# Kernel optimization log

Hardware: AMD Instinct MI355X
Metric: run time of the kernel (lower is better)

Reference implementation:

```python
import jax, jax.numpy as jnp
import numpy as np

N_NODES = 50000
N_EDGES = 1600000
D_IN = 128
D_HID = 128
D_OUT = 128


def setup_inputs() -> dict:
    key = jax.random.key(0)
    ks = jax.random.split(key, 12)
    s = 0.05
    return {
        "x": jax.random.normal(ks[0], (N_NODES, D_IN), jnp.float32),
        "src": jax.random.randint(ks[1], (N_EDGES,), 0, N_NODES),
        "dst": jax.random.randint(ks[2], (N_EDGES,), 0, N_NODES),
        "W_neigh1": jax.random.normal(ks[3], (D_HID, D_IN), jnp.float32) * s,
        "W_self1": jax.random.normal(ks[4], (D_HID, D_IN), jnp.float32) * s,
        "b_self1": jnp.zeros((D_HID,), jnp.float32),
        "W_neigh2": jax.random.normal(ks[5], (D_HID, D_HID), jnp.float32) * s,
        "W_self2": jax.random.normal(ks[6], (D_HID, D_HID), jnp.float32) * s,
        "b_self2": jnp.zeros((D_HID,), jnp.float32),
        "W_neigh3": jax.random.normal(ks[7], (D_OUT, D_HID), jnp.float32) * s,
        "W_self3": jax.random.normal(ks[8], (D_OUT, D_HID), jnp.float32) * s,
        "b_self3": jnp.zeros((D_OUT,), jnp.float32),
    }


def _sage_mean(h, src, dst, inv_deg, W_neigh, W_self, b_self):
    # DGL SAGEConv 'mean': fc_self(h) + fc_neigh(mean of in-neighbor feats)
    # zero in-degree nodes get zero neighbor term (inv_deg = 0 there is avoided
    # by clamping degree to >=1, sum is 0 anyway).
    neigh_sum = jax.ops.segment_sum(h[src], dst, num_segments=h.shape[0])  # [N, d]
    h_neigh = neigh_sum * inv_deg  # [N, d]
    return h @ W_self.T + b_self + h_neigh @ W_neigh.T


def reference(x, src, dst, W_neigh1, W_self1, b_self1, W_neigh2, W_self2, b_self2, W_neigh3, W_self3, b_self3):
    n = x.shape[0]
    deg = jax.ops.segment_sum(jnp.ones((src.shape[0],), x.dtype), dst, num_segments=n)
    inv_deg = (1.0 / jnp.maximum(deg, 1.0))[:, None]  # [N, 1]
    h = jax.nn.relu(_sage_mean(x, src, dst, inv_deg, W_neigh1, W_self1, b_self1))
    h = jax.nn.relu(_sage_mean(h, src, dst, inv_deg, W_neigh2, W_self2, b_self2))
    h = _sage_mean(h, src, dst, inv_deg, W_neigh3, W_self3, b_self3)
    return h
```

## Files before the change

kernel.cpp:

```cpp
#include <hip/hip_runtime.h>


constexpr int N_NODES = 50000;
constexpr int N_EDGES = 1600000;
constexpr int D = 128;
constexpr int NTILES = N_NODES / 16;

constexpr int NBUCK = 392;
constexpr int BCAP  = 6144;
constexpr int EPB   = 4096;
constexpr int CS_BLOCKS = (N_EDGES + EPB - 1) / EPB;
constexpr int GC_STRIDE = 16;

constexpr int NT  = 8;
constexpr int TSH = 13;

typedef __bf16 bf16x8 __attribute__((ext_vector_type(8)));
typedef float f32x4 __attribute__((ext_vector_type(4)));
union U8 { bf16x8 v; __bf16 e[8]; };

__global__ __launch_bounds__(256) void bucket_count_scatter(
        const int* __restrict__ dst, const int* __restrict__ src,
        int* __restrict__ gcursor, int* __restrict__ bucketbuf) {
    __shared__ int hcnt[NBUCK];
    __shared__ int hbase[NBUCK];
    const int tid = threadIdx.x;
    for (int i = tid; i < NBUCK; i += 256) hcnt[i] = 0;
    __syncthreads();

    const int e0 = blockIdx.x * EPB;
    int d[16], lp[16];
    #pragma unroll
    for (int t = 0; t < 16; ++t) {
        const int e = e0 + t * 256 + tid;
        if (e < N_EDGES) {
            d[t] = dst[e];
            lp[t] = atomicAdd(&hcnt[d[t] >> 7], 1);
        } else {
            d[t] = 0; lp[t] = -1;
        }
    }
    __syncthreads();

    for (int i = tid; i < NBUCK; i += 256) {
        const int c = hcnt[i];
        hbase[i] = c ? atomicAdd(&gcursor[i * GC_STRIDE], c) : 0;
    }
    __syncthreads();

    #pragma unroll
    for (int t = 0; t < 16; ++t) {
        const int e = e0 + t * 256 + tid;
        if (e < N_EDGES) {
            const int s  = src[e];
            const int bk = d[t] >> 7;
            const int p  = hbase[bk] + lp[t];
            if (p < BCAP)
                bucketbuf[bk * BCAP + p] = ((d[t] & 127) << 16) | s;
        }
    }
}

__global__ __launch_bounds__(256) void bucket_csr(
        const int* __restrict__ gcursor, const int* __restrict__ bucketbuf,
        int* __restrict__ tp, float* __restrict__ inv_deg,
        int* __restrict__ esrc) {
    __shared__ int h[1024];
    __shared__ int cur[1024];
    __shared__ int wsum[4], wpre[4];
    __shared__ int redw[4];
    const int bk = blockIdx.x, tid = threadIdx.x;
    int cnt = gcursor[bk * GC_STRIDE];
    if (cnt > BCAP) cnt = BCAP;

    int partial = 0;
    for (int i = tid; i < bk; i += 256) {
        int v = gcursor[i * GC_STRIDE];
        partial += (v > BCAP ? BCAP : v);
    }
    #pragma unroll
    for (int off = 32; off; off >>= 1) partial += __shfl_down(partial, off, 64);
    if ((tid & 63) == 0) redw[tid >> 6] = partial;

    #pragma unroll
    for (int k = 0; k < 4; ++k) h[tid * 4 + k] = 0;
    __syncthreads();
    const int base = redw[0] + redw[1] + redw[2] + redw[3];

    const int* bb = bucketbuf + (size_t)bk * BCAP;
    for (int i = tid; i < cnt; i += 256) {
        const int p = bb[i];
        atomicAdd(&h[((p >> 16) << 3) | ((p & 0xFFFF) >> TSH)], 1);
    }
    __syncthreads();

    if (tid < 128) {
        int dg = 0;
        #pragma unroll
        for (int k = 0; k < 8; ++k) dg += h[tid * 8 + k];
        inv_deg[bk * 128 + tid] = 1.0f / fmaxf((float)dg, 1.0f);
    }

    const int v0 = h[tid * 4], v1 = h[tid * 4 + 1];
    const int v2 = h[tid * 4 + 2], v3 = h[tid * 4 + 3];
    const int s = v0 + v1 + v2 + v3;
    int x = s;
    const int lane = tid & 63, w = tid >> 6;
    #pragma unroll
    for (int off = 1; off < 64; off <<= 1) {
        int tt = __shfl_up(x, off, 64);
        if (lane >= off) x += tt;
    }
    if (lane == 63) wsum[w] = x;
    __syncthreads();
    if (tid == 0) {
        int a = 0;
        #pragma unroll
        for (int k = 0; k < 4; ++k) { wpre[k] = a; a += wsum[k]; }
    }
    __syncthreads();
    const int e0 = wpre[w] + (x - s);
    const int e1 = e0 + v0, e2 = e1 + v1, e3 = e2 + v2;
    cur[tid * 4] = e0; cur[tid * 4 + 1] = e1;
    cur[tid * 4 + 2] = e2; cur[tid * 4 + 3] = e3;
    int* tpo = tp + (size_t)bk * 1024 + tid * 4;
    tpo[0] = base + e0; tpo[1] = base + e1; tpo[2] = base + e2; tpo[3] = base + e3;
    __syncthreads();

    for (int i = tid; i < cnt; i += 256) {
        const int p = bb[i];
        const int f = ((p >> 16) << 3) | ((p & 0xFFFF) >> TSH);
        esrc[base + atomicAdd(&cur[f], 1)] = p & 0xFFFF;
    }
}

__global__ void pack_w(const float* __restrict__ w0, const float* __restrict__ w1,
                       const float* __restrict__ w2, const float* __restrict__ w3,
                       const float* __restrict__ w4, const float* __restrict__ w5,
                       __bf16* __restrict__ outbase) {
    const float* ws[6] = {w0, w1, w2, w3, w4, w5};
    const float* W = ws[blockIdx.y];
    __bf16* o = outbase + (size_t)blockIdx.y * 32768;
    int idx = blockIdx.x * 256 + threadIdx.x;
    int t = idx & 7;
    int lane = (idx >> 3) & 63;
    int ks = (idx >> 9) & 3;
    int jt = idx >> 11;
    int j = jt * 16 + (lane & 15);
    int k = ks * 32 + (lane >> 4) * 8 + t;
    float w = W[j * D + k];
    __bf16 hi = (__bf16)w;
    o[idx] = hi;
    o[16384 + idx] = (__bf16)(w - (float)hi);
}

__global__ __launch_bounds__(256) void split_x(const float* __restrict__ x,
                                               __bf16* __restrict__ xh, int n8) {
    const int i = blockIdx.x * 256 + threadIdx.x;
    if (i < n8) {
        const float* p = x + (size_t)i * 8;
        const f32x4 a = *(const f32x4*)p;
        const f32x4 b = *(const f32x4*)(p + 4);
        U8 h;
        #pragma unroll
        for (int k = 0; k < 4; ++k) { h.e[k] = (__bf16)a[k]; h.e[4 + k] = (__bf16)b[k]; }
        *(bf16x8*)(xh + (size_t)i * 8) = h.v;
    }
}

__global__ __launch_bounds__(256) void agg_mean(
        const __bf16* __restrict__ hplane, const int* __restrict__ esrc,
        const int* __restrict__ tp, const float* __restrict__ inv_deg,
        __bf16* __restrict__ m_hi, __bf16* __restrict__ m_lo) {
    const int n = blockIdx.x * 4 + (threadIdx.x >> 6);
    const int lane = threadIdx.x & 63;
    const int s = lane >> 4;
    const int c = lane & 15;
    const int r0 = tp[n * NT], r1 = tp[(n + 1) * NT];

    float acc[8] = {0.f, 0.f, 0.f, 0.f, 0.f, 0.f, 0.f, 0.f};
    int e = r0 + s;
    for (; e + 12 < r1; e += 16) {
        int i0 = esrc[e], i1 = esrc[e + 4], i2 = esrc[e + 8], i3 = esrc[e + 12];
        U8 v0, v1, v2, v3;
        v0.v = *(const bf16x8*)(hplane + (size_t)i0 * D + c * 8);
        v1.v = *(const bf16x8*)(hplane + (size_t)i1 * D + c * 8);
        v2.v = *(const bf16x8*)(hplane + (size_t)i2 * D + c * 8);
        v3.v = *(const bf16x8*)(hplane + (size_t)i3 * D + c * 8);
        #pragma unroll
        for (int t = 0; t < 8; ++t)
            acc[t] += ((float)v0.e[t] + (float)v1.e[t]) + ((float)v2.e[t] + (float)v3.e[t]);
    }
    for (; e < r1; e += 4) {
        U8 v0;
        v0.v = *(const bf16x8*)(hplane + (size_t)esrc[e] * D + c * 8);
        #pragma unroll
        for (int t = 0; t < 8; ++t) acc[t] += (float)v0.e[t];
    }
    #pragma unroll
    for (int t = 0; t < 8; ++t) acc[t] += __shfl_down(acc[t], 32, 64);
    #pragma unroll
    for (int t = 0; t < 8; ++t) acc[t] += __shfl_down(acc[t], 16, 64);

    if (lane < 16) {
        const float idg = inv_deg[n];
        U8 mh, ml;
        #pragma unroll
        for (int t = 0; t < 8; ++t) {
            const float mm = acc[t] * idg;
            const __bf16 hi = (__bf16)mm;
            mh.e[t] = hi;
            ml.e[t] = (__bf16)(mm - (float)hi);
        }
        *(bf16x8*)(m_hi + (size_t)n * D + c * 8) = mh.v;
        *(bf16x8*)(m_lo + (size_t)n * D + c * 8) = ml.v;
    }
}

__global__ __launch_bounds__(256) void fused_gemm(
        const float* __restrict__ x32,
        const __bf16* __restrict__ a_hi, const __bf16* __restrict__ a_lo,
        const __bf16* __restrict__ m_hi, const __bf16* __restrict__ m_lo,
        const __bf16* __restrict__ Bs, const __bf16* __restrict__ Bn,
        const float* __restrict__ bias,
        __bf16* __restrict__ o_hi, __bf16* __restrict__ o_lo,
        float* __restrict__ o32) {
    const int wave = threadIdx.x >> 6;
    const int lane = threadIdx.x & 63;
    const int tile = blockIdx.x;
    const int n0 = tile * 16;
    const int row = n0 + (lane & 15);
    const int koff = (lane >> 4) * 8;

    U8 ah[4], al[4], mh[4], ml[4];
    if (x32) {
        #pragma unroll
        for (int ks = 0; ks < 4; ++ks) {
            const float* p = x32 + (size_t)row * D + ks * 32 + koff;
            float f[8];
            *(f32x4*)&f[0] = *(const f32x4*)p;
            *(f32x4*)&f[4] = *(const f32x4*)(p + 4);
            #pragma unroll
            for (int t = 0; t < 8; ++t) {
                const __bf16 hi = (__bf16)f[t];
                ah[ks].e[t] = hi;
                al[ks].e[t] = (__bf16)(f[t] - (float)hi);
            }
        }
    } else {
        #pragma unroll
        for (int ks = 0; ks < 4; ++ks) {
            ah[ks].v = *(const bf16x8*)(a_hi + (size_t)row * D + ks * 32 + koff);
            al[ks].v = *(const bf16x8*)(a_lo + (size_t)row * D + ks * 32 + koff);
        }
    }
    #pragma unroll
    for (int ks = 0; ks < 4; ++ks) {
        mh[ks].v = *(const bf16x8*)(m_hi + (size_t)row * D + ks * 32 + koff);
        ml[ks].v = *(const bf16x8*)(m_lo + (size_t)row * D + ks * 32 + koff);
    }

    const int jcol = lane & 15;
    const int r0q = (lane >> 4) * 4;

    #pragma unroll
    for (int jj = 0; jj < 2; ++jj) {
        const int jt = wave * 2 + jj;
        f32x4 accS = {0.f, 0.f, 0.f, 0.f};
        f32x4 accN = {0.f, 0.f, 0.f, 0.f};
        #pragma unroll
        for (int ks = 0; ks < 4; ++ks) {
            const size_t off = (((size_t)jt * 4 + ks) * 64 + lane) * 8;
            const bf16x8 wsh = *(const bf16x8*)(Bs + off);
            const bf16x8 wsl = *(const bf16x8*)(Bs + 16384 + off);
            const bf16x8 wnh = *(const bf16x8*)(Bn + off);
            const bf16x8 wnl = *(const bf16x8*)(Bn + 16384 + off);
            accS = __builtin_amdgcn_mfma_f32_16x16x32_bf16(ah[ks].v, wsh, accS, 0, 0, 0);
            accS = __builtin_amdgcn_mfma_f32_16x16x32_bf16(al[ks].v, wsh, accS, 0, 0, 0);
            accS = __builtin_amdgcn_mfma_f32_16x16x32_bf16(ah[ks].v, wsl, accS, 0, 0, 0);
            accN = __builtin_amdgcn_mfma_f32_16x16x32_bf16(mh[ks].v, wnh, accN, 0, 0, 0);
            accN = __builtin_amdgcn_mfma_f32_16x16x32_bf16(ml[ks].v, wnh, accN, 0, 0, 0);
            accN = __builtin_amdgcn_mfma_f32_16x16x32_bf16(mh[ks].v, wnl, accN, 0, 0, 0);
        }
        const int j = jt * 16 + jcol;
        const float bj = bias[j];
        if (o32) {
            #pragma unroll
            for (int r = 0; r < 4; ++r) {
                const size_t n = n0 + r0q + r;
                o32[n * D + j] = accS[r] + accN[r] + bj;
            }
        } else {
            #pragma unroll
            for (int r = 0; r < 4; ++r) {
                const size_t n = n0 + r0q + r;
                float o = fmaxf(accS[r] + accN[r] + bj, 0.f);
                const __bf16 hi = (__bf16)o;
                o_hi[n * D + j] = hi;
                o_lo[n * D + j] = (__bf16)(o - (float)hi);
            }
        }
    }
}

extern "C" void kernel_launch(void* const* d_in, const int* in_sizes, int n_in,
                              void* d_out, int out_size, void* d_ws, size_t ws_size,
                              hipStream_t stream) {
    const float* x   = (const float*)d_in[0];
    const int* src   = (const int*)d_in[1];
    const int* dst   = (const int*)d_in[2];
    const float* Wn1 = (const float*)d_in[3];
    const float* Ws1 = (const float*)d_in[4];
    const float* b1  = (const float*)d_in[5];
    const float* Wn2 = (const float*)d_in[6];
    const float* Ws2 = (const float*)d_in[7];
    const float* b2  = (const float*)d_in[8];
    const float* Wn3 = (const float*)d_in[9];
    const float* Ws3 = (const float*)d_in[10];
    const float* b3  = (const float*)d_in[11];
    float* out = (float*)d_out;

    constexpr size_t PLANE = (size_t)50176 * D * 2;

    char* w = (char*)d_ws;
    float* inv_deg = (float*)w;                 w += 50176 * 4;
    int* tp        = (int*)w;                   w += (size_t)NBUCK * 1024 * 4;
    int* gcursor   = (int*)w;                   w += NBUCK * GC_STRIDE * 4;
    int* esrc      = (int*)w;                   w += (size_t)N_EDGES * 4;
    __bf16* Bpk    = (__bf16*)w;                w += 6 * 32768 * 2;
    __bf16* xh     = (__bf16*)w;                w += PLANE;
    __bf16* mhi    = (__bf16*)w;                w += PLANE;
    __bf16* mlo    = (__bf16*)w;                w += PLANE;
    __bf16* pAh    = (__bf16*)w;                w += PLANE;
    __bf16* pAl    = (__bf16*)w;                w += PLANE;
    __bf16* pBh    = (__bf16*)w;                w += PLANE;
    __bf16* pBl    = (__bf16*)w;

    int* bucketbuf = (int*)pBh;

    const __bf16* PWs1 = Bpk + 0 * 32768, *PWn1 = Bpk + 1 * 32768;
    const __bf16* PWs2 = Bpk + 2 * 32768, *PWn2 = Bpk + 3 * 32768;
    const __bf16* PWs3 = Bpk + 4 * 32768, *PWn3 = Bpk + 5 * 32768;

    hipMemsetAsync(gcursor, 0, NBUCK * GC_STRIDE * 4, stream);
    bucket_count_scatter<<<CS_BLOCKS, 256, 0, stream>>>(dst, src, gcursor, bucketbuf);
    bucket_csr<<<NBUCK, 256, 0, stream>>>(gcursor, bucketbuf, tp, inv_deg, esrc);

    pack_w<<<dim3(64, 6), 256, 0, stream>>>(Ws1, Wn1, Ws2, Wn2, Ws3, Wn3, Bpk);
    split_x<<<(N_NODES * D / 8 + 255) / 256, 256, 0, stream>>>(x, xh, N_NODES * D / 8);

    const int agrid = N_NODES / 4;

    agg_mean<<<agrid, 256, 0, stream>>>(xh, esrc, tp, inv_deg, mhi, mlo);
    fused_gemm<<<NTILES, 256, 0, stream>>>(x, nullptr, nullptr, mhi, mlo,
                                           PWs1, PWn1, b1, pAh, pAl, nullptr);

    agg_mean<<<agrid, 256, 0, stream>>>(pAh, esrc, tp, inv_deg, mhi, mlo);
    fused_gemm<<<NTILES, 256, 0, stream>>>(nullptr, pAh, pAl, mhi, mlo,
                                           PWs2, PWn2, b2, pBh, pBl, nullptr);

    agg_mean<<<agrid, 256, 0, stream>>>(pBh, esrc, tp, inv_deg, mhi, mlo);
    fused_gemm<<<NTILES, 256, 0, stream>>>(nullptr, pBh, pBl, mhi, mlo,
                                           PWs3, PWn3, b3, nullptr, nullptr, out);
}
```

Baseline: 424.1 us.

## Fuse neighbor mean aggregation into per-tile GEMM kernel via LDS

Result: slower. 440.2 us (+3.8%).

```diff
diff --git a/kernel.cpp b/kernel.cpp
--- a/kernel.cpp
+++ b/kernel.cpp
@@ -14,6 +14,9 @@
 
 constexpr int NT  = 8;
 constexpr int TSH = 13;
+
+constexpr int LROW = 272;
+constexpr int LPLANE = 16 * LROW;
 
 typedef __bf16 bf16x8 __attribute__((ext_vector_type(8)));
 typedef float f32x4 __attribute__((ext_vector_type(4)));
@@ -168,75 +171,76 @@
     }
 }
 
-__global__ __launch_bounds__(256) void agg_mean(
-        const __bf16* __restrict__ hplane, const int* __restrict__ esrc,
-        const int* __restrict__ tp, const float* __restrict__ inv_deg,
-        __bf16* __restrict__ m_hi, __bf16* __restrict__ m_lo) {
-    const int n = blockIdx.x * 4 + (threadIdx.x >> 6);
-    const int lane = threadIdx.x & 63;
-    const int s = lane >> 4;
-    const int c = lane & 15;
-    const int r0 = tp[n * NT], r1 = tp[(n + 1) * NT];
-
-    float acc[8] = {0.f, 0.f, 0.f, 0.f, 0.f, 0.f, 0.f, 0.f};
-    int e = r0 + s;
-    for (; e + 12 < r1; e += 16) {
-        int i0 = esrc[e], i1 = esrc[e + 4], i2 = esrc[e + 8], i3 = esrc[e + 12];
-        U8 v0, v1, v2, v3;
-        v0.v = *(const bf16x8*)(hplane + (size_t)i0 * D + c * 8);
-        v1.v = *(const bf16x8*)(hplane + (size_t)i1 * D + c * 8);
-        v2.v = *(const bf16x8*)(hplane + (size_t)i2 * D + c * 8);
-        v3.v = *(const bf16x8*)(hplane + (size_t)i3 * D + c * 8);
-        #pragma unroll
-        for (int t = 0; t < 8; ++t)
-            acc[t] += ((float)v0.e[t] + (float)v1.e[t]) + ((float)v2.e[t] + (float)v3.e[t]);
-    }
-    for (; e < r1; e += 4) {
-        U8 v0;
-        v0.v = *(const bf16x8*)(hplane + (size_t)esrc[e] * D + c * 8);
-        #pragma unroll
-        for (int t = 0; t < 8; ++t) acc[t] += (float)v0.e[t];
-    }
-    #pragma unroll
-    for (int t = 0; t < 8; ++t) acc[t] += __shfl_down(acc[t], 32, 64);
-    #pragma unroll
-    for (int t = 0; t < 8; ++t) acc[t] += __shfl_down(acc[t], 16, 64);
-
-    if (lane < 16) {
-        const float idg = inv_deg[n];
-        U8 mh, ml;
-        #pragma unroll
-        for (int t = 0; t < 8; ++t) {
-            const float mm = acc[t] * idg;
-            const __bf16 hi = (__bf16)mm;
-            mh.e[t] = hi;
-            ml.e[t] = (__bf16)(mm - (float)hi);
-        }
-        *(bf16x8*)(m_hi + (size_t)n * D + c * 8) = mh.v;
-        *(bf16x8*)(m_lo + (size_t)n * D + c * 8) = ml.v;
-    }
-}
-
-__global__ __launch_bounds__(256) void fused_gemm(
+__global__ __launch_bounds__(256) void fused_layer(
         const float* __restrict__ x32,
         const __bf16* __restrict__ a_hi, const __bf16* __restrict__ a_lo,
-        const __bf16* __restrict__ m_hi, const __bf16* __restrict__ m_lo,
+        const __bf16* __restrict__ g_hi,
+        const int* __restrict__ esrc, const int* __restrict__ tp,
+        const float* __restrict__ inv_deg,
         const __bf16* __restrict__ Bs, const __bf16* __restrict__ Bn,
         const float* __restrict__ bias,
         __bf16* __restrict__ o_hi, __bf16* __restrict__ o_lo,
         float* __restrict__ o32) {
+    __shared__ __attribute__((aligned(16))) char lm[2 * LPLANE];
     const int wave = threadIdx.x >> 6;
     const int lane = threadIdx.x & 63;
-    const int tile = blockIdx.x;
-    const int n0 = tile * 16;
-    const int row = n0 + (lane & 15);
-    const int koff = (lane >> 4) * 8;
+    const int n0 = blockIdx.x * 16;
+    const int s = lane >> 4;
+    const int c = lane & 15;
+
+    for (int i = 0; i < 4; ++i) {
+        const int r = wave * 4 + i;
+        const int n = n0 + r;
+        const int r0 = tp[n * NT], r1 = tp[(n + 1) * NT];
+
+        float acc[8] = {0.f, 0.f, 0.f, 0.f, 0.f, 0.f, 0.f, 0.f};
+        int e = r0 + s;
+        for (; e + 12 < r1; e += 16) {
+            int i0 = esrc[e], i1 = esrc[e + 4], i2 = esrc[e + 8], i3 = esrc[e + 12];
+            U8 v0, v1, v2, v3;
+            v0.v = *(const bf16x8*)(g_hi + (size_t)i0 * D + c * 8);
+            v1.v = *(const bf16x8*)(g_hi + (size_t)i1 * D + c * 8);
+            v2.v = *(const bf16x8*)(g_hi + (size_t)i2 * D + c * 8);
+            v3.v = *(const bf16x8*)(g_hi + (size_t)i3 * D + c * 8);
+            #pragma unroll
+            for (int t = 0; t < 8; ++t)
+                acc[t] += ((float)v0.e[t] + (float)v1.e[t]) + ((float)v2.e[t] + (float)v3.e[t]);
+        }
+        for (; e < r1; e += 4) {
+            U8 v0;
+            v0.v = *(const bf16x8*)(g_hi + (size_t)esrc[e] * D + c * 8);
+            #pragma unroll
+            for (int t = 0; t < 8; ++t) acc[t] += (float)v0.e[t];
+        }
+        #pragma unroll
+        for (int t = 0; t < 8; ++t) acc[t] += __shfl_down(acc[t], 32, 64);
+        #pragma unroll
+        for (int t = 0; t < 8; ++t) acc[t] += __shfl_down(acc[t], 16, 64);
+
+        if (lane < 16) {
+            const float idg = inv_deg[n];
+            U8 mh, ml;
+            #pragma unroll
+            for (int t = 0; t < 8; ++t) {
+                const float mm = acc[t] * idg;
+                const __bf16 hi = (__bf16)mm;
+                mh.e[t] = hi;
+                ml.e[t] = (__bf16)(mm - (float)hi);
+            }
+            *(bf16x8*)(lm + r * LROW + c * 16) = mh.v;
+            *(bf16x8*)(lm + LPLANE + r * LROW + c * 16) = ml.v;
+        }
+    }
+    __syncthreads();
+
+    const int row = n0 + c;
+    const int ko8 = (lane >> 4) * 8;
 
     U8 ah[4], al[4], mh[4], ml[4];
     if (x32) {
         #pragma unroll
         for (int ks = 0; ks < 4; ++ks) {
-            const float* p = x32 + (size_t)row * D + ks * 32 + koff;
+            const float* p = x32 + (size_t)row * D + ks * 32 + ko8;
             float f[8];
             *(f32x4*)&f[0] = *(const f32x4*)p;
             *(f32x4*)&f[4] = *(const f32x4*)(p + 4);
@@ -250,17 +254,17 @@
     } else {
         #pragma unroll
         for (int ks = 0; ks < 4; ++ks) {
-            ah[ks].v = *(const bf16x8*)(a_hi + (size_t)row * D + ks * 32 + koff);
-            al[ks].v = *(const bf16x8*)(a_lo + (size_t)row * D + ks * 32 + koff);
+            ah[ks].v = *(const bf16x8*)(a_hi + (size_t)row * D + ks * 32 + ko8);
+            al[ks].v = *(const bf16x8*)(a_lo + (size_t)row * D + ks * 32 + ko8);
         }
     }
     #pragma unroll
     for (int ks = 0; ks < 4; ++ks) {
-        mh[ks].v = *(const bf16x8*)(m_hi + (size_t)row * D + ks * 32 + koff);
-        ml[ks].v = *(const bf16x8*)(m_lo + (size_t)row * D + ks * 32 + koff);
-    }
-
-    const int jcol = lane & 15;
+        const int lb = c * LROW + ks * 64 + (lane >> 4) * 16;
+        mh[ks].v = *(const bf16x8*)(lm + lb);
+        ml[ks].v = *(const bf16x8*)(lm + LPLANE + lb);
+    }
+
     const int r0q = (lane >> 4) * 4;
 
     #pragma unroll
@@ -282,7 +286,7 @@
             accN = __builtin_amdgcn_mfma_f32_16x16x32_bf16(ml[ks].v, wnh, accN, 0, 0, 0);
             accN = __builtin_amdgcn_mfma_f32_16x16x32_bf16(mh[ks].v, wnl, accN, 0, 0, 0);
         }
-        const int j = jt * 16 + jcol;
+        const int j = jt * 16 + c;
         const float bj = bias[j];
         if (o32) {
             #pragma unroll
@@ -329,8 +333,6 @@
     int* esrc      = (int*)w;                   w += (size_t)N_EDGES * 4;
     __bf16* Bpk    = (__bf16*)w;                w += 6 * 32768 * 2;
     __bf16* xh     = (__bf16*)w;                w += PLANE;
-    __bf16* mhi    = (__bf16*)w;                w += PLANE;
-    __bf16* mlo    = (__bf16*)w;                w += PLANE;
     __bf16* pAh    = (__bf16*)w;                w += PLANE;
     __bf16* pAl    = (__bf16*)w;                w += PLANE;
     __bf16* pBh    = (__bf16*)w;                w += PLANE;
@@ -349,17 +351,15 @@
     pack_w<<<dim3(64, 6), 256, 0, stream>>>(Ws1, Wn1, Ws2, Wn2, Ws3, Wn3, Bpk);
     split_x<<<(N_NODES * D / 8 + 255) / 256, 256, 0, stream>>>(x, xh, N_NODES * D / 8);
 
-    const int agrid = N_NODES / 4;
-
-    agg_mean<<<agrid, 256, 0, stream>>>(xh, esrc, tp, inv_deg, mhi, mlo);
-    fused_gemm<<<NTILES, 256, 0, stream>>>(x, nullptr, nullptr, mhi, mlo,
-                                           PWs1, PWn1, b1, pAh, pAl, nullptr);
-
-    agg_mean<<<agrid, 256, 0, stream>>>(pAh, esrc, tp, inv_deg, mhi, mlo);
-    fused_gemm<<<NTILES, 256, 0, stream>>>(nullptr, pAh, pAl, mhi, mlo,
-                                           PWs2, PWn2, b2, pBh, pBl, nullptr);
-
-    agg_mean<<<agrid, 256, 0, stream>>>(pBh, esrc, tp, inv_deg, mhi, mlo);
-    fused_gemm<<<NTILES, 256, 0, stream>>>(nullptr, pBh, pBl, mhi, mlo,
-                                           PWs3, PWn3, b3, nullptr, nullptr, out);
-}
+    fused_layer<<<NTILES, 256, 0, stream>>>(x, nullptr, nullptr, xh,
+                                            esrc, tp, inv_deg,
+                                            PWs1, PWn1, b1, pAh, pAl, nullptr);
+
+    fused_layer<<<NTILES, 256, 0, stream>>>(nullptr, pAh, pAl, pAh,
+                                            esrc, tp, inv_deg,
+                                            PWs2, PWn2, b2, pBh, pBl, nullptr);
+
+    fused_layer<<<NTILES, 256, 0, stream>>>(nullptr, pBh, pBl, pBh,
+                                            esrc, tp, inv_deg,
+                                            PWs3, PWn3, b3, nullptr, nullptr, out);
+}
```
